# Optimization experiments

Measured on AMD Instinct MI355X. Metric: run time of the kernel, lower is better.

The kernel has to match this reference:

```python
import jax, jax.numpy as jnp
import numpy as np

B, D_IN, D_OUT, DICT = 2048, 768, 768, 24576
TOP_K, TOP_K_AUX = 32, 512
L1_COEFF, AUX_PENALTY, N_DEAD = 0.001, 0.03125, 100.0


def setup_inputs() -> dict:
    key = jax.random.key(0)
    k1, k2, k3, k4, k5, k6 = jax.random.split(key, 6)
    x_in = jax.random.normal(k1, (B, D_IN), dtype=jnp.float32)
    y_target = jax.random.normal(k2, (B, D_OUT), dtype=jnp.float32)
    nb = jax.random.randint(k3, (DICT,), 0, 200).astype(jnp.float32)
    # kaiming-uniform-ish init
    bound_e = float(np.sqrt(6.0 / D_IN))
    W_enc = jax.random.uniform(k4, (D_IN, DICT), minval=-bound_e, maxval=bound_e, dtype=jnp.float32)
    bound_d = float(np.sqrt(6.0 / DICT))
    W_dec = jax.random.uniform(k5, (DICT, D_OUT), minval=-bound_d, maxval=bound_d, dtype=jnp.float32)
    W_dec = W_dec / jnp.linalg.norm(W_dec, axis=-1, keepdims=True)  # unit-norm rows
    b_dec = jnp.zeros((D_OUT,), dtype=jnp.float32)
    return {"x_in": x_in, "y_target": y_target, "num_batches_not_active": nb,
            "W_enc": W_enc, "W_dec": W_dec, "b_dec": b_dec}


def _unit_norm(x):
    m = x.mean(axis=-1, keepdims=True)
    x = x - m
    s = jnp.std(x, axis=-1, keepdims=True, ddof=1)  # torch .std is unbiased
    return x / (s + 1e-5), m, s


def reference(x_in, y_target, num_batches_not_active, W_enc, W_dec, b_dec):
    xn, _, _ = _unit_norm(x_in)
    yn, y_mean, y_std = _unit_norm(y_target)
    x_enc = xn - b_dec  # pre_enc_bias (input_size == output_size)
    acts = jax.nn.relu(x_enc @ W_enc)                      # [B, DICT]
    vals, idx = jax.lax.top_k(acts, TOP_K)                 # [B, TOP_K]
    rows = jnp.arange(B)[:, None]
    acts_sparse = jnp.zeros_like(acts).at[rows, idx].set(vals)
    y_pred = acts_sparse @ W_dec + b_dec                   # [B, D_OUT]
    y_pred_out = y_pred * y_std + y_mean

    # stateful dead-feature bookkeeping (update_inactive_features)
    col_active = acts_sparse.sum(axis=0) > 0
    nb = jnp.where(col_active, 0.0, num_batches_not_active + 1.0)

    l2_loss = jnp.mean((y_pred - yn) ** 2)
    l1_norm = jnp.mean(jnp.abs(acts_sparse).sum(axis=-1))
    l1_loss = L1_COEFF * l1_norm
    l0_norm = jnp.mean((acts_sparse > 0).astype(jnp.float32).sum(axis=-1))

    # auxiliary loss on dead features (static-shape masked top-k; masked cols
    # get -1 < relu acts so extras relu-clip to 0 -> same math as torch gather)
    dead = nb >= N_DEAD
    masked = jnp.where(dead[None, :], acts, -1.0)
    av, ai = jax.lax.top_k(masked, TOP_K_AUX)
    av = jax.nn.relu(av)
    acts_aux = jnp.zeros_like(acts).at[rows, ai].set(av)
    y_pred_aux = acts_aux @ W_dec
    residual = yn - y_pred
    l2_aux = AUX_PENALTY * jnp.mean((y_pred_aux - residual) ** 2)
    aux_loss = jnp.where(dead.any(), l2_aux, 0.0)

    loss = l2_loss + l1_loss + aux_loss
    num_dead_features = (nb > N_DEAD).sum()
    return (y_pred_out, acts_sparse, loss, l2_loss, l1_loss, l0_norm, l1_norm,
            aux_loss, num_dead_features)
```

## Files before the change

kernel.cpp:

```cpp
#include <hip/hip_runtime.h>
#include <math.h>

#define BATCH 2048
#define DIN 768
#define DICT 24576
#define KM 32
#define KA 512
#define NPT 48
#define L1_COEFF 0.001f
#define AUX_PENALTY 0.03125f
#define CAND_MAX 128
#define CAND_DELTA 0.08f
#define AUXC (KA + 64)

typedef __attribute__((ext_vector_type(8))) short bf16x8;
typedef __attribute__((ext_vector_type(8))) unsigned short u16x8;
typedef __attribute__((ext_vector_type(4))) float f32x4;

constexpr size_t WS_XENC   = 0;
constexpr size_t WS_YN     = WS_XENC + (size_t)BATCH*DIN;
constexpr size_t WS_YMEAN  = WS_YN + (size_t)BATCH*DIN;
constexpr size_t WS_YSTD   = WS_YMEAN + BATCH;
constexpr size_t WS_RES    = WS_YSTD + BATCH;
constexpr size_t WS_NSEL   = WS_RES + (size_t)BATCH*DIN;
constexpr size_t WS_SEL    = WS_NSEL + BATCH;
constexpr size_t WS_SELV   = WS_SEL + (size_t)BATCH*KM;
constexpr size_t WS_COLACT = WS_SELV + (size_t)BATCH*KM;
constexpr size_t WS_ACC    = WS_COLACT + DICT;
constexpr size_t WS_DB     = WS_ACC + 8;
constexpr size_t WS_XEB    = WS_DB + DICT/32;
constexpr size_t WS_WETF   = WS_XEB + (size_t)BATCH*DIN/2;
constexpr size_t WS_WETB   = WS_WETF + (size_t)DICT*DIN;
constexpr size_t WS_WDB    = WS_WETB + (size_t)DICT*DIN/2;

__device__ __forceinline__ unsigned short f2b(float f){
    unsigned u = __float_as_uint(f);
    return (unsigned short)((u + 0x7fffu + ((u >> 16) & 1u)) >> 16);
}
__device__ __forceinline__ float b2f(unsigned short h){ return __uint_as_float(((unsigned)h) << 16); }

__device__ __forceinline__ void gld_lds16(const void* g, void* l){
    __builtin_amdgcn_global_load_lds(
        (const __attribute__((address_space(1))) unsigned int*)g,
        (__attribute__((address_space(3))) unsigned int*)l, 16, 0, 0);
}

__device__ __forceinline__ int blk_count512(int c, int* s16, int par){
    #pragma unroll
    for (int off=32; off; off>>=1) c += __shfl_down(c, off);
    if ((threadIdx.x & 63) == 0) s16[par*8 + (threadIdx.x >> 6)] = c;
    __syncthreads();
    int tot = 0;
    #pragma unroll
    for (int w=0; w<8; w++) tot += s16[par*8+w];
    return tot;
}
__device__ __forceinline__ float blk_sum512(float v, float* s16, int par){
    #pragma unroll
    for (int off=32; off; off>>=1) v += __shfl_down(v, off);
    if ((threadIdx.x & 63) == 0) s16[par*8 + (threadIdx.x >> 6)] = v;
    __syncthreads();
    float t = 0.f;
    #pragma unroll
    for (int w=0; w<8; w++) t += s16[par*8+w];
    return t;
}
__device__ __forceinline__ float blk_sum256(float v, float* s8, int par){
    #pragma unroll
    for (int off=32; off; off>>=1) v += __shfl_down(v, off);
    if ((threadIdx.x & 63) == 0) s8[par*4 + (threadIdx.x >> 6)] = v;
    __syncthreads();
    float t = 0.f;
    #pragma unroll
    for (int w=0; w<4; w++) t += s8[par*4+w];
    return t;
}

__global__ __launch_bounds__(256) void normalize_k(const float* __restrict__ x,
        const float* __restrict__ y, const float* __restrict__ bdec,
        float* __restrict__ ws){
    __shared__ float s8[8];
    int b = blockIdx.x; bool isy = b >= BATCH; int row = isy ? b - BATCH : b;
    const float* src = (isy ? y : x) + (size_t)row*DIN;
    int tid = threadIdx.x;
    float v0 = src[tid], v1 = src[tid+256], v2 = src[tid+512];
    float s = blk_sum256(v0+v1+v2, s8, 0);
    float mean = s * (1.f/(float)DIN);
    float d0 = v0-mean, d1 = v1-mean, d2 = v2-mean;
    float vs = blk_sum256(d0*d0+d1*d1+d2*d2, s8, 1);
    float sd = sqrtf(vs / (float)(DIN-1));
    float inv = 1.f / (sd + 1e-5f);
    if (isy){
        float* yn = ws + WS_YN + (size_t)row*DIN;
        yn[tid] = d0*inv; yn[tid+256] = d1*inv; yn[tid+512] = d2*inv;
        if (tid==0){ ws[WS_YMEAN+row] = mean; ws[WS_YSTD+row] = sd; }
    } else {
        float* xe = ws + WS_XENC + (size_t)row*DIN;
        unsigned short* xeb = (unsigned short*)(ws + WS_XEB) + (size_t)row*DIN;
        float e0 = d0*inv - bdec[tid];
        float e1 = d1*inv - bdec[tid+256];
        float e2 = d2*inv - bdec[tid+512];
        xe[tid] = e0; xe[tid+256] = e1; xe[tid+512] = e2;
        xeb[tid] = f2b(e0); xeb[tid+256] = f2b(e1); xeb[tid+512] = f2b(e2);
    }
}

__global__ __launch_bounds__(256) void transpose_k(const float* __restrict__ W,
        float* __restrict__ Tf, unsigned short* __restrict__ Tb){
    __shared__ float t[32][33];
    int n0 = blockIdx.x*32, k0 = blockIdx.y*32;
    int r = threadIdx.x >> 5, c = threadIdx.x & 31;
    #pragma unroll
    for (int rr=r; rr<32; rr+=8) t[rr][c] = W[(size_t)(k0+rr)*DICT + n0 + c];
    __syncthreads();
    #pragma unroll
    for (int rr=r; rr<32; rr+=8){
        float v = t[c][rr];
        Tf[(size_t)(n0+rr)*DIN + k0 + c] = v;
        Tb[(size_t)(n0+rr)*DIN + k0 + c] = f2b(v);
    }
}

__global__ __launch_bounds__(256) void wdecb_k(const float* __restrict__ W,
        unsigned short* __restrict__ Wb){
    size_t n4 = (size_t)DICT*DIN/4;
    for (size_t i = (size_t)blockIdx.x*256 + threadIdx.x; i < n4; i += (size_t)gridDim.x*256){
        float4 v = ((const float4*)W)[i];
        ushort4 o; o.x=f2b(v.x); o.y=f2b(v.y); o.z=f2b(v.z); o.w=f2b(v.w);
        ((ushort4*)Wb)[i] = o;
    }
}

__global__ __launch_bounds__(256) void gemm_mfma(const unsigned short* __restrict__ Abf,
        const unsigned short* __restrict__ Bbf, unsigned short* __restrict__ C){
    __shared__ __align__(16) unsigned short As[128*64];
    __shared__ __align__(16) unsigned short Bs[128*64];
    const int tid = threadIdx.x;
    const int w = tid >> 6, lane = tid & 63;
    const int m0 = blockIdx.y*128, n0 = blockIdx.x*128;
    const int srow = lane >> 3;
    const int schunk = (lane & 7) ^ srow;
    const int wm = (w >> 1)*64, wn = (w & 1)*64;
    f32x4 acc[16];
    #pragma unroll
    for (int i=0;i<16;i++) acc[i] = (f32x4){0.f,0.f,0.f,0.f};
    for (int kt = 0; kt < DIN; kt += 64){
        #pragma unroll
        for (int q=0;q<4;q++){
            int s = w*4 + q;
            int row = 8*s + srow;
            gld_lds16(Abf + (size_t)(m0+row)*DIN + kt + schunk*8, &As[8*s*64]);
            gld_lds16(Bbf + (size_t)(n0+row)*DIN + kt + schunk*8, &Bs[8*s*64]);
        }
        __syncthreads();
        #pragma unroll
        for (int kk=0; kk<64; kk+=32){
            bf16x8 af[4], bfr[4];
            int ch = (kk>>3) + (lane>>4);
            #pragma unroll
            for (int i=0;i<4;i++){
                int row = wm + i*16 + (lane&15);
                af[i] = *(const bf16x8*)&As[row*64 + ((ch ^ (row&7))<<3)];
            }
            #pragma unroll
            for (int j=0;j<4;j++){
                int row = wn + j*16 + (lane&15);
                bfr[j] = *(const bf16x8*)&Bs[row*64 + ((ch ^ (row&7))<<3)];
            }
            #pragma unroll
            for (int i=0;i<4;i++)
                #pragma unroll
                for (int j=0;j<4;j++)
                    acc[i*4+j] = __builtin_amdgcn_mfma_f32_16x16x32_bf16(af[i], bfr[j], acc[i*4+j], 0,0,0);
        }
        __syncthreads();
    }
    #pragma unroll
    for (int i=0;i<4;i++){
        #pragma unroll
        for (int r=0;r<4;r++){
            int m = m0 + wm + i*16 + (lane>>4)*4 + r;
            unsigned short* crow = C + (size_t)m*DICT + n0 + wn + (lane&15);
            #pragma unroll
            for (int j=0;j<4;j++)
                crow[j*16] = f2b(fmaxf(acc[i*4+j][r], 0.f) + 0.0f);
        }
    }
}

__global__ __launch_bounds__(512) void topk_main(const unsigned short* __restrict__ actsb,
        const float* __restrict__ WeTf, const float* __restrict__ Wdec,
        const float* __restrict__ bdec, float* __restrict__ ws,
        float* __restrict__ ypred_out){
    const int row = blockIdx.x, tid = threadIdx.x;
    const int lane = tid & 63, wid = tid >> 6;
    __shared__ int   s_i16[16];
    __shared__ float s_f16[16];
    __shared__ float s_x[DIN];
    __shared__ int   s_ci[CAND_MAX];
    __shared__ float s_cv[CAND_MAX];
    __shared__ int   s_li[KM];
    __shared__ float s_lv[KM];
    __shared__ int   s_n, s_m;
    const unsigned short* arow = actsb + (size_t)row * DICT;
    const float* xrow = ws + WS_XENC + (size_t)row * DIN;
    unsigned short h[NPT];
    #pragma unroll
    for (int i=0;i<6;i++){
        u16x8 v = *(const u16x8*)&arow[i*4096 + tid*8];
        #pragma unroll
        for (int e=0;e<8;e++) h[i*8+e] = v[e];
    }
    s_x[tid] = xrow[tid];
    if (tid < DIN-512) s_x[tid+512] = xrow[tid+512];
    if (tid == 0){ s_n = 0; s_m = 0; }

    int par = 0;
    unsigned prefix = 0;
    for (int bit=14; bit>=0; bit--){
        unsigned cand = prefix | (1u<<bit);
        int c = 0;
        #pragma unroll
        for (int q=0;q<NPT;q++) c += ((unsigned)h[q] >= cand) ? 1 : 0;
        int tot = blk_count512(c, s_i16, par); par ^= 1;
        if (tot >= KM) prefix = cand;
    }
    float tc = b2f((unsigned short)prefix) - CAND_DELTA;
    #pragma unroll
    for (int q=0;q<NPT;q++){
        if (b2f(h[q]) > tc){
            int p = atomicAdd(&s_n, 1);
            if (p < CAND_MAX) s_ci[p] = (q>>3)*4096 + tid*8 + (q&7);
        }
    }
    __syncthreads();
    int nc = s_n; if (nc > CAND_MAX) nc = CAND_MAX;
    for (int c = wid; c < nc; c += 8){
        const float* wr = WeTf + (size_t)s_ci[c]*DIN;
        float p = 0.f;
        #pragma unroll
        for (int t=0; t<12; t++) p = fmaf(s_x[lane + 64*t], wr[lane + 64*t], p);
        #pragma unroll
        for (int off=32; off; off>>=1) p += __shfl_down(p, off);
        if (lane == 0) s_cv[c] = fmaxf(p, 0.f);
    }
    __syncthreads();
    if (tid < nc){
        float vi = s_cv[tid]; int ii = s_ci[tid];
        int rank = 0;
        for (int j=0; j<nc; j++){
            float vj = s_cv[j];
            rank += (vj > vi) || (vj == vi && s_ci[j] < ii);
        }
        if (rank < KM){
            int p = atomicAdd(&s_m, 1);
            s_li[p] = ii; s_lv[p] = vi;
        }
    }
    __syncthreads();
    if (tid < KM){
        ((int*)ws)[WS_COLACT + s_li[tid]] = 1;
        ((int*)ws)[WS_SEL  + (size_t)row*KM + tid] = s_li[tid];
        ws[WS_SELV + (size_t)row*KM + tid] = s_lv[tid];
    }
    if (tid == 0){
        float l1 = 0.f; int l0 = 0;
        for (int l=0;l<KM;l++){ l1 += s_lv[l]; l0 += (s_lv[l] > 0.f); }
        atomicAdd(&ws[WS_ACC+1], l1);
        atomicAdd(&ws[WS_ACC+2], (float)l0);
    }
    __syncthreads();
    float ym = ws[WS_YMEAN+row], ys = ws[WS_YSTD+row];
    float l2loc = 0.f;
    for (int c = tid; c < DIN; c += 512){
        float acc = bdec[c];
        #pragma unroll 4
        for (int l=0;l<KM;l++) acc = fmaf(s_lv[l], Wdec[(size_t)s_li[l]*DIN + c], acc);
        float ynv = ws[WS_YN + (size_t)row*DIN + c];
        float d = acc - ynv;
        l2loc += d*d;
        ws[WS_RES + (size_t)row*DIN + c] = ynv - acc;
        ypred_out[(size_t)row*DIN + c] = fmaf(acc, ys, ym);
    }
    float l2t = blk_sum512(l2loc, s_f16, 0);
    if (tid==0) atomicAdd(&ws[WS_ACC+0], l2t);
}

__global__ __launch_bounds__(256) void dead_update(const float* __restrict__ nb,
        float* __restrict__ ws){
    int j = blockIdx.x*256 + threadIdx.x;
    int lane = threadIdx.x & 63;
    int act = ((const int*)ws)[WS_COLACT + j];
    float nbn = act ? 0.f : nb[j] + 1.f;
    bool dead = nbn >= 100.0f;
    unsigned long long bal = __ballot(dead ? 1 : 0);
    if (lane == 0){
        unsigned* db = (unsigned*)(ws + WS_DB);
        int w = j >> 5;
        db[w]   = (unsigned)bal;
        db[w+1] = (unsigned)(bal >> 32);
        if (bal) atomicOr(((int*)ws) + WS_ACC + 5, 1);
    }
    int c = (nbn > 100.0f) ? 1 : 0;
    #pragma unroll
    for (int off=32; off; off>>=1) c += __shfl_down(c, off);
    if (lane == 0 && c) atomicAdd(&ws[WS_ACC+4], (float)c);
}

__global__ __launch_bounds__(512) void aux_k(const unsigned short* __restrict__ actsb,
        const unsigned short* __restrict__ WdB, float* __restrict__ ws){
    const int row = blockIdx.x, tid = threadIdx.x;
    const int lane = tid & 63, wid = tid >> 6;
    __shared__ int      s_i16[16];
    __shared__ float    s_f16[16];
    __shared__ unsigned s_db[DICT/32];
    __shared__ int      s_li[AUXC];
    __shared__ float    s_lv[AUXC];
    __shared__ int      s_n;
    __shared__ float    s_red[8*DIN];
    const unsigned short* arow = actsb + (size_t)row * DICT;

    for (int i=tid; i<DICT/32; i+=512) s_db[i] = ((const unsigned*)(ws + WS_DB))[i];
    if (tid==0) s_n = 0;
    __syncthreads();

    unsigned short key[NPT];
    #pragma unroll
    for (int i=0;i<6;i++){
        u16x8 v = *(const u16x8*)&arow[i*4096 + tid*8];
        unsigned byte = (s_db[i*128 + (tid>>2)] >> ((tid&3)*8)) & 0xFFu;
        #pragma unroll
        for (int e=0;e<8;e++){
            unsigned short hv = v[e];
            key[i*8+e] = (((byte>>e)&1u) && hv) ? hv : 0;
        }
    }

    int par = 0;
    unsigned prefix = 0;
    for (int bit=14; bit>=0; bit--){
        unsigned cand = prefix | (1u<<bit);
        int c = 0;
        #pragma unroll
        for (int q=0;q<NPT;q++) c += ((unsigned)key[q] >= cand) ? 1 : 0;
        int tot = blk_count512(c, s_i16, par); par ^= 1;
        if (tot >= KA) prefix = cand;
    }
    unsigned thr = prefix ? prefix : 1u;
    #pragma unroll
    for (int q=0;q<NPT;q++){
        if ((unsigned)key[q] >= thr){
            int p = atomicAdd(&s_n, 1);
            if (p < AUXC){
                s_li[p] = (q>>3)*4096 + tid*8 + (q&7);
                s_lv[p] = b2f(key[q]);
            }
        }
    }
    __syncthreads();
    int n = s_n; if (n > AUXC) n = AUXC;

    float a[12];
    #pragma unroll
    for (int i=0;i<12;i++) a[i] = 0.f;
    const int base = lane*12;
    for (int l = wid; l < n; l += 8){
        float v = s_lv[l];
        const unsigned short* wr = WdB + (size_t)s_li[l]*DIN + base;
        ushort4 q0 = *(const ushort4*)wr;
        ushort4 q1 = *(const ushort4*)(wr+4);
        ushort4 q2 = *(const ushort4*)(wr+8);
        a[0] = fmaf(v, b2f(q0.x), a[0]); a[1] = fmaf(v, b2f(q0.y), a[1]);
        a[2] = fmaf(v, b2f(q0.z), a[2]); a[3] = fmaf(v, b2f(q0.w), a[3]);
        a[4] = fmaf(v, b2f(q1.x), a[4]); a[5] = fmaf(v, b2f(q1.y), a[5]);
        a[6] = fmaf(v, b2f(q1.z), a[6]); a[7] = fmaf(v, b2f(q1.w), a[7]);
        a[8] = fmaf(v, b2f(q2.x), a[8]); a[9] = fmaf(v, b2f(q2.y), a[9]);
        a[10]= fmaf(v, b2f(q2.z), a[10]); a[11]= fmaf(v, b2f(q2.w), a[11]);
    }
    float* pr = &s_red[wid*DIN + base];
    *(float4*)pr     = make_float4(a[0],a[1],a[2],a[3]);
    *(float4*)(pr+4) = make_float4(a[4],a[5],a[6],a[7]);
    *(float4*)(pr+8) = make_float4(a[8],a[9],a[10],a[11]);
    __syncthreads();
    float ss = 0.f;
    for (int c = tid; c < DIN; c += 512){
        float s = 0.f;
        #pragma unroll
        for (int w=0; w<8; w++) s += s_red[w*DIN + c];
        float d = s - ws[WS_RES + (size_t)row*DIN + c];
        ss += d*d;
    }
    float tot = blk_sum512(ss, s_f16, 0);
    if (tid==0) atomicAdd(&ws[WS_ACC+3], tot);
}

__global__ __launch_bounds__(256) void zscatter(const float* __restrict__ ws,
        float* __restrict__ acts){
    const int row = blockIdx.x, tid = threadIdx.x;
    float4 z = make_float4(0.f,0.f,0.f,0.f);
    float4* arow4 = (float4*)(acts + (size_t)row*DICT);
    #pragma unroll
    for (int i=0;i<24;i++) arow4[tid + 256*i] = z;
    __syncthreads();
    if (tid < KM){
        int j   = ((const int*)ws)[WS_SEL + (size_t)row*KM + tid];
        float v = ws[WS_SELV + (size_t)row*KM + tid];
        (acts + (size_t)row*DICT)[j] = v;
    }
}

__global__ void finalize_k(const float* __restrict__ ws, float* __restrict__ out){
    if (threadIdx.x == 0){
        float l2   = ws[WS_ACC+0] / (float)((size_t)BATCH*DIN);
        float l1n  = ws[WS_ACC+1] / (float)BATCH;
        float l1l  = L1_COEFF * l1n;
        float l0   = ws[WS_ACC+2] / (float)BATCH;
        float auxm = AUX_PENALTY * (ws[WS_ACC+3] / (float)((size_t)BATCH*DIN));
        int any    = ((const int*)ws)[WS_ACC+5];
        float auxl = any ? auxm : 0.f;
        out[0] = l2 + l1l + auxl;
        out[1] = l2;
        out[2] = l1l;
        out[3] = l0;
        out[4] = l1n;
        out[5] = auxl;
        out[6] = ws[WS_ACC+4];
    }
}

extern "C" void kernel_launch(void* const* d_in, const int* in_sizes, int n_in,
                              void* d_out, int out_size, void* d_ws, size_t ws_size,
                              hipStream_t stream){
    const float* x_in = (const float*)d_in[0];
    const float* y_t  = (const float*)d_in[1];
    const float* nb   = (const float*)d_in[2];
    const float* Wenc = (const float*)d_in[3];
    const float* Wdec = (const float*)d_in[4];
    const float* bdec = (const float*)d_in[5];
    float* out  = (float*)d_out;
    float* ws   = (float*)d_ws;
    float* acts = out + (size_t)BATCH*DIN;
    float* scal = out + (size_t)BATCH*DIN + (size_t)BATCH*DICT;
    unsigned short* actsb = (unsigned short*)acts;

    unsigned short* xeb  = (unsigned short*)(ws + WS_XEB);
    float*          wetf = ws + WS_WETF;
    unsigned short* wetb = (unsigned short*)(ws + WS_WETB);
    unsigned short* wdb  = (unsigned short*)(ws + WS_WDB);

    hipMemsetAsync(ws + WS_COLACT, 0, (DICT + 8) * sizeof(float), stream);
    normalize_k<<<2*BATCH, 256, 0, stream>>>(x_in, y_t, bdec, ws);
    transpose_k<<<dim3(DICT/32, DIN/32), 256, 0, stream>>>(Wenc, wetf, wetb);
    wdecb_k<<<2048, 256, 0, stream>>>(Wdec, wdb);
    gemm_mfma<<<dim3(DICT/128, BATCH/128), 256, 0, stream>>>(xeb, wetb, actsb);
    topk_main<<<BATCH, 512, 0, stream>>>(actsb, wetf, Wdec, bdec, ws, out);
    dead_update<<<DICT/256, 256, 0, stream>>>(nb, ws);
    aux_k<<<BATCH, 512, 0, stream>>>(actsb, wdb, ws);
    zscatter<<<BATCH, 256, 0, stream>>>(ws, acts);
    finalize_k<<<1, 64, 0, stream>>>(ws, scal);
}
```

Before: 838.9 us.

## Replace per-row aux gather-FMA with compacted dead-column MFMA GEMM

The auxiliary loss path now works only on dead columns. A prefix scan over the dead bitmask compacts both the per-row activations and a transposed bf16 W_dec down to those columns. The aux product then runs as a split-K MFMA GEMM that accumulates with atomics, followed by a separate loss-reduction kernel. This replaces the scattered per-row row-gathers of W_dec with dense tensor-core work. It adds several small kernels, a transpose and a memset, plus float atomic contention. The radix top-k count loops also switch to ballot/popcount wave counting.

Result: no change. 855.6 us (+2.0%).

```diff
diff --git a/kernel.cpp b/kernel.cpp
--- a/kernel.cpp
+++ b/kernel.cpp
@@ -11,7 +11,7 @@
 #define AUX_PENALTY 0.03125f
 #define CAND_MAX 128
 #define CAND_DELTA 0.08f
-#define AUXC (KA + 64)
+#define AUX_SPLIT 8
 
 typedef __attribute__((ext_vector_type(8))) short bf16x8;
 typedef __attribute__((ext_vector_type(8))) unsigned short u16x8;
@@ -32,6 +32,9 @@
 constexpr size_t WS_WETF   = WS_XEB + (size_t)BATCH*DIN/2;
 constexpr size_t WS_WETB   = WS_WETF + (size_t)DICT*DIN;
 constexpr size_t WS_WDB    = WS_WETB + (size_t)DICT*DIN/2;
+constexpr size_t WS_DCNT   = WS_XEB;
+constexpr size_t WS_DPREF  = WS_XEB + DICT/32;
+constexpr size_t WS_META   = WS_XEB + 2*(DICT/32);
 
 __device__ __forceinline__ unsigned short f2b(float f){
     unsigned u = __float_as_uint(f);
@@ -45,10 +48,8 @@
         (__attribute__((address_space(3))) unsigned int*)l, 16, 0, 0);
 }
 
-__device__ __forceinline__ int blk_count512(int c, int* s16, int par){
-    #pragma unroll
-    for (int off=32; off; off>>=1) c += __shfl_down(c, off);
-    if ((threadIdx.x & 63) == 0) s16[par*8 + (threadIdx.x >> 6)] = c;
+__device__ __forceinline__ int blk_count512_w(int cw, int* s16, int par){
+    if ((threadIdx.x & 63) == 0) s16[par*8 + (threadIdx.x >> 6)] = cw;
     __syncthreads();
     int tot = 0;
     #pragma unroll
@@ -121,14 +122,17 @@
     }
 }
 
-__global__ __launch_bounds__(256) void wdecb_k(const float* __restrict__ W,
-        unsigned short* __restrict__ Wb){
-    size_t n4 = (size_t)DICT*DIN/4;
-    for (size_t i = (size_t)blockIdx.x*256 + threadIdx.x; i < n4; i += (size_t)gridDim.x*256){
-        float4 v = ((const float4*)W)[i];
-        ushort4 o; o.x=f2b(v.x); o.y=f2b(v.y); o.z=f2b(v.z); o.w=f2b(v.w);
-        ((ushort4*)Wb)[i] = o;
-    }
+__global__ __launch_bounds__(256) void wdect_k(const float* __restrict__ W,
+        unsigned short* __restrict__ T){
+    __shared__ float t[32][33];
+    int j0 = blockIdx.x*32, n0 = blockIdx.y*32;
+    int r = threadIdx.x >> 5, c = threadIdx.x & 31;
+    #pragma unroll
+    for (int rr=r; rr<32; rr+=8) t[rr][c] = W[(size_t)(j0+rr)*DIN + n0 + c];
+    __syncthreads();
+    #pragma unroll
+    for (int rr=r; rr<32; rr+=8)
+        T[(size_t)(n0+rr)*DICT + j0 + c] = f2b(t[c][rr]);
 }
 
 __global__ __launch_bounds__(256) void gemm_mfma(const unsigned short* __restrict__ Abf,
@@ -221,8 +225,8 @@
         unsigned cand = prefix | (1u<<bit);
         int c = 0;
         #pragma unroll
-        for (int q=0;q<NPT;q++) c += ((unsigned)h[q] >= cand) ? 1 : 0;
-        int tot = blk_count512(c, s_i16, par); par ^= 1;
+        for (int q=0;q<NPT;q++) c += (int)__popcll(__ballot((unsigned)h[q] >= cand));
+        int tot = blk_count512_w(c, s_i16, par); par ^= 1;
         if (tot >= KM) prefix = cand;
     }
     float tc = b2f((unsigned short)prefix) - CAND_DELTA;
@@ -296,9 +300,12 @@
     unsigned long long bal = __ballot(dead ? 1 : 0);
     if (lane == 0){
         unsigned* db = (unsigned*)(ws + WS_DB);
+        int* dc = (int*)(ws + WS_DCNT);
         int w = j >> 5;
         db[w]   = (unsigned)bal;
         db[w+1] = (unsigned)(bal >> 32);
+        dc[w]   = __popc((unsigned)bal);
+        dc[w+1] = __popc((unsigned)(bal >> 32));
         if (bal) atomicOr(((int*)ws) + WS_ACC + 5, 1);
     }
     int c = (nbn > 100.0f) ? 1 : 0;
@@ -307,32 +314,91 @@
     if (lane == 0 && c) atomicAdd(&ws[WS_ACC+4], (float)c);
 }
 
-__global__ __launch_bounds__(512) void aux_k(const unsigned short* __restrict__ actsb,
-        const unsigned short* __restrict__ WdB, float* __restrict__ ws){
+__global__ __launch_bounds__(256) void scan_k(float* __restrict__ ws){
+    __shared__ int s[DICT/32];
+    const int* dc = (const int*)(ws + WS_DCNT);
+    int tid = threadIdx.x;
+    for (int i=tid; i<DICT/32; i+=256) s[i] = dc[i];
+    __syncthreads();
+    for (int off=1; off<DICT/32; off<<=1){
+        int v[3];
+        #pragma unroll
+        for (int k=0;k<3;k++){ int i = tid + 256*k; v[k] = (i >= off) ? s[i-off] : 0; }
+        __syncthreads();
+        #pragma unroll
+        for (int k=0;k<3;k++){ int i = tid + 256*k; s[i] += v[k]; }
+        __syncthreads();
+    }
+    int* dp = (int*)(ws + WS_DPREF);
+    for (int i=tid; i<DICT/32; i+=256) dp[i] = s[i] - dc[i];
+    if (tid == 0){
+        int nd = s[DICT/32 - 1];
+        int ndpad = (nd + 63) & ~63;
+        int nkt = ndpad >> 6;
+        int* meta = (int*)(ws + WS_META);
+        meta[0] = nd; meta[1] = ndpad; meta[2] = nkt;
+        meta[3] = (nkt + AUX_SPLIT - 1) / AUX_SPLIT;
+    }
+}
+
+__global__ __launch_bounds__(256) void wdtcompact_k(float* __restrict__ ws,
+        unsigned short* __restrict__ wdt){
+    __shared__ unsigned s_db[DICT/32];
+    __shared__ int      s_dp[DICT/32];
+    const int tid = threadIdx.x, n = blockIdx.x;
+    for (int i=tid; i<DICT/32; i+=256){
+        s_db[i] = ((const unsigned*)(ws + WS_DB))[i];
+        s_dp[i] = ((const int*)(ws + WS_DPREF))[i];
+    }
+    const int nd    = ((const int*)(ws + WS_META))[0];
+    const int ndpad = ((const int*)(ws + WS_META))[1];
+    __syncthreads();
+    unsigned short* row = wdt + (size_t)n*DICT;
+    for (int ch = 0; ch < DICT; ch += 4096){
+        unsigned short v[16];
+        u16x8 a = *(const u16x8*)&row[ch + tid*16];
+        u16x8 b = *(const u16x8*)&row[ch + tid*16 + 8];
+        #pragma unroll
+        for (int e=0;e<8;e++){ v[e] = a[e]; v[8+e] = b[e]; }
+        __syncthreads();
+        int w = (ch>>5) + (tid>>1);
+        unsigned dbw = s_db[w]; int dpw = s_dp[w];
+        int bit0 = (tid&1)*16;
+        #pragma unroll
+        for (int e=0;e<16;e++){
+            int bit = bit0 + e;
+            if ((dbw >> bit) & 1u)
+                row[dpw + __popc(dbw & ((1u<<bit)-1u))] = v[e];
+        }
+        __syncthreads();
+    }
+    for (int t = nd + tid; t < ndpad; t += 256) row[t] = 0;
+}
+
+__global__ __launch_bounds__(512) void aux_select(unsigned short* __restrict__ actsb,
+        float* __restrict__ ws){
     const int row = blockIdx.x, tid = threadIdx.x;
-    const int lane = tid & 63, wid = tid >> 6;
     __shared__ int      s_i16[16];
-    __shared__ float    s_f16[16];
     __shared__ unsigned s_db[DICT/32];
-    __shared__ int      s_li[AUXC];
-    __shared__ float    s_lv[AUXC];
-    __shared__ int      s_n;
-    __shared__ float    s_red[8*DIN];
-    const unsigned short* arow = actsb + (size_t)row * DICT;
-
-    for (int i=tid; i<DICT/32; i+=512) s_db[i] = ((const unsigned*)(ws + WS_DB))[i];
-    if (tid==0) s_n = 0;
+    __shared__ int      s_dp[DICT/32];
+    unsigned short* arow = actsb + (size_t)row * DICT;
+    for (int i=tid; i<DICT/32; i+=512){
+        s_db[i] = ((const unsigned*)(ws + WS_DB))[i];
+        s_dp[i] = ((const int*)(ws + WS_DPREF))[i];
+    }
+    const int nd    = ((const int*)(ws + WS_META))[0];
+    const int ndpad = ((const int*)(ws + WS_META))[1];
     __syncthreads();
 
     unsigned short key[NPT];
     #pragma unroll
     for (int i=0;i<6;i++){
         u16x8 v = *(const u16x8*)&arow[i*4096 + tid*8];
-        unsigned byte = (s_db[i*128 + (tid>>2)] >> ((tid&3)*8)) & 0xFFu;
+        unsigned dbw = s_db[i*128 + (tid>>2)];
         #pragma unroll
         for (int e=0;e<8;e++){
             unsigned short hv = v[e];
-            key[i*8+e] = (((byte>>e)&1u) && hv) ? hv : 0;
+            key[i*8+e] = (((dbw >> ((tid&3)*8 + e)) & 1u) && hv) ? hv : 0;
         }
     }
 
@@ -342,56 +408,107 @@
         unsigned cand = prefix | (1u<<bit);
         int c = 0;
         #pragma unroll
-        for (int q=0;q<NPT;q++) c += ((unsigned)key[q] >= cand) ? 1 : 0;
-        int tot = blk_count512(c, s_i16, par); par ^= 1;
+        for (int q=0;q<NPT;q++) c += (int)__popcll(__ballot((unsigned)key[q] >= cand));
+        int tot = blk_count512_w(c, s_i16, par); par ^= 1;
         if (tot >= KA) prefix = cand;
     }
     unsigned thr = prefix ? prefix : 1u;
-    #pragma unroll
-    for (int q=0;q<NPT;q++){
-        if ((unsigned)key[q] >= thr){
-            int p = atomicAdd(&s_n, 1);
-            if (p < AUXC){
-                s_li[p] = (q>>3)*4096 + tid*8 + (q&7);
-                s_lv[p] = b2f(key[q]);
+
+    #pragma unroll
+    for (int i=0;i<6;i++){
+        int w = i*128 + (tid>>2);
+        unsigned dbw = s_db[w];
+        int dpw = s_dp[w];
+        #pragma unroll
+        for (int e=0;e<8;e++){
+            int bit = (tid&3)*8 + e;
+            if ((dbw >> bit) & 1u){
+                int p = dpw + __popc(dbw & ((1u<<bit)-1u));
+                unsigned short kv = key[i*8+e];
+                arow[p] = ((unsigned)kv >= thr) ? kv : (unsigned short)0;
             }
         }
     }
-    __syncthreads();
-    int n = s_n; if (n > AUXC) n = AUXC;
-
-    float a[12];
-    #pragma unroll
-    for (int i=0;i<12;i++) a[i] = 0.f;
-    const int base = lane*12;
-    for (int l = wid; l < n; l += 8){
-        float v = s_lv[l];
-        const unsigned short* wr = WdB + (size_t)s_li[l]*DIN + base;
-        ushort4 q0 = *(const ushort4*)wr;
-        ushort4 q1 = *(const ushort4*)(wr+4);
-        ushort4 q2 = *(const ushort4*)(wr+8);
-        a[0] = fmaf(v, b2f(q0.x), a[0]); a[1] = fmaf(v, b2f(q0.y), a[1]);
-        a[2] = fmaf(v, b2f(q0.z), a[2]); a[3] = fmaf(v, b2f(q0.w), a[3]);
-        a[4] = fmaf(v, b2f(q1.x), a[4]); a[5] = fmaf(v, b2f(q1.y), a[5]);
-        a[6] = fmaf(v, b2f(q1.z), a[6]); a[7] = fmaf(v, b2f(q1.w), a[7]);
-        a[8] = fmaf(v, b2f(q2.x), a[8]); a[9] = fmaf(v, b2f(q2.y), a[9]);
-        a[10]= fmaf(v, b2f(q2.z), a[10]); a[11]= fmaf(v, b2f(q2.w), a[11]);
-    }
-    float* pr = &s_red[wid*DIN + base];
-    *(float4*)pr     = make_float4(a[0],a[1],a[2],a[3]);
-    *(float4*)(pr+4) = make_float4(a[4],a[5],a[6],a[7]);
-    *(float4*)(pr+8) = make_float4(a[8],a[9],a[10],a[11]);
-    __syncthreads();
-    float ss = 0.f;
-    for (int c = tid; c < DIN; c += 512){
-        float s = 0.f;
-        #pragma unroll
-        for (int w=0; w<8; w++) s += s_red[w*DIN + c];
-        float d = s - ws[WS_RES + (size_t)row*DIN + c];
-        ss += d*d;
-    }
-    float tot = blk_sum512(ss, s_f16, 0);
-    if (tid==0) atomicAdd(&ws[WS_ACC+3], tot);
+    for (int t = nd + tid; t < ndpad; t += 512) arow[t] = 0;
+}
+
+__global__ __launch_bounds__(256) void aux_gemm(const unsigned short* __restrict__ Abf,
+        const unsigned short* __restrict__ Bbf, const float* __restrict__ ws,
+        float* __restrict__ yaux){
+    const int nkt   = ((const int*)(ws + WS_META))[2];
+    const int chunk = ((const int*)(ws + WS_META))[3];
+    int t0 = blockIdx.z * chunk;
+    int t1 = t0 + chunk; if (t1 > nkt) t1 = nkt;
+    if (t0 >= t1) return;
+    __shared__ __align__(16) unsigned short As[128*64];
+    __shared__ __align__(16) unsigned short Bs[128*64];
+    const int tid = threadIdx.x;
+    const int w = tid >> 6, lane = tid & 63;
+    const int m0 = blockIdx.y*128, n0 = blockIdx.x*128;
+    const int srow = lane >> 3;
+    const int schunk = (lane & 7) ^ srow;
+    const int wm = (w >> 1)*64, wn = (w & 1)*64;
+    f32x4 acc[16];
+    #pragma unroll
+    for (int i=0;i<16;i++) acc[i] = (f32x4){0.f,0.f,0.f,0.f};
+    for (int t = t0; t < t1; ++t){
+        int kt = t*64;
+        #pragma unroll
+        for (int q=0;q<4;q++){
+            int s = w*4 + q;
+            int row = 8*s + srow;
+            gld_lds16(Abf + (size_t)(m0+row)*DICT + kt + schunk*8, &As[8*s*64]);
+            gld_lds16(Bbf + (size_t)(n0+row)*DICT + kt + schunk*8, &Bs[8*s*64]);
+        }
+        __syncthreads();
+        #pragma unroll
+        for (int kk=0; kk<64; kk+=32){
+            bf16x8 af[4], bfr[4];
+            int ch = (kk>>3) + (lane>>4);
+            #pragma unroll
+            for (int i=0;i<4;i++){
+                int row = wm + i*16 + (lane&15);
+                af[i] = *(const bf16x8*)&As[row*64 + ((ch ^ (row&7))<<3)];
+            }
+            #pragma unroll
+            for (int j=0;j<4;j++){
+                int row = wn + j*16 + (lane&15);
+                bfr[j] = *(const bf16x8*)&Bs[row*64 + ((ch ^ (row&7))<<3)];
+            }
+            #pragma unroll
+            for (int i=0;i<4;i++)
+                #pragma unroll
+                for (int j=0;j<4;j++)
+                    acc[i*4+j] = __builtin_amdgcn_mfma_f32_16x16x32_bf16(af[i], bfr[j], acc[i*4+j], 0,0,0);
+        }
+        __syncthreads();
+    }
+    #pragma unroll
+    for (int i=0;i<4;i++){
+        #pragma unroll
+        for (int r=0;r<4;r++){
+            int m = m0 + wm + i*16 + (lane>>4)*4 + r;
+            float* crow = yaux + (size_t)m*DIN + n0 + wn + (lane&15);
+            #pragma unroll
+            for (int j=0;j<4;j++) atomicAdd(&crow[j*16], acc[i*4+j][r]);
+        }
+    }
+}
+
+__global__ __launch_bounds__(256) void auxloss_k(const float* __restrict__ yaux,
+        float* __restrict__ ws){
+    __shared__ float s8[8];
+    const float4* y4 = (const float4*)yaux;
+    const float4* r4 = (const float4*)(ws + WS_RES);
+    float s = 0.f;
+    const size_t n4 = (size_t)BATCH*DIN/4;
+    for (size_t i = (size_t)blockIdx.x*256 + threadIdx.x; i < n4; i += (size_t)gridDim.x*256){
+        float4 a = y4[i], b = r4[i];
+        float d0 = a.x-b.x, d1 = a.y-b.y, d2 = a.z-b.z, d3 = a.w-b.w;
+        s += d0*d0 + d1*d1 + d2*d2 + d3*d3;
+    }
+    float tot = blk_sum256(s, s8, 0);
+    if (threadIdx.x == 0) atomicAdd(&ws[WS_ACC+3], tot);
 }
 
 __global__ __launch_bounds__(256) void zscatter(const float* __restrict__ ws,
@@ -446,16 +563,22 @@
     unsigned short* xeb  = (unsigned short*)(ws + WS_XEB);
     float*          wetf = ws + WS_WETF;
     unsigned short* wetb = (unsigned short*)(ws + WS_WETB);
-    unsigned short* wdb  = (unsigned short*)(ws + WS_WDB);
+    unsigned short* wdt  = (unsigned short*)(ws + WS_WDB);
+    float*          yaux = ws + WS_XENC;
 
     hipMemsetAsync(ws + WS_COLACT, 0, (DICT + 8) * sizeof(float), stream);
     normalize_k<<<2*BATCH, 256, 0, stream>>>(x_in, y_t, bdec, ws);
     transpose_k<<<dim3(DICT/32, DIN/32), 256, 0, stream>>>(Wenc, wetf, wetb);
-    wdecb_k<<<2048, 256, 0, stream>>>(Wdec, wdb);
+    wdect_k<<<dim3(DICT/32, DIN/32), 256, 0, stream>>>(Wdec, wdt);
     gemm_mfma<<<dim3(DICT/128, BATCH/128), 256, 0, stream>>>(xeb, wetb, actsb);
     topk_main<<<BATCH, 512, 0, stream>>>(actsb, wetf, Wdec, bdec, ws, out);
+    hipMemsetAsync(yaux, 0, (size_t)BATCH*DIN*sizeof(float), stream);
     dead_update<<<DICT/256, 256, 0, stream>>>(nb, ws);
-    aux_k<<<BATCH, 512, 0, stream>>>(actsb, wdb, ws);
+    scan_k<<<1, 256, 0, stream>>>(ws);
+    wdtcompact_k<<<DIN, 256, 0, stream>>>(ws, wdt);
+    aux_select<<<BATCH, 512, 0, stream>>>(actsb, ws);
+    aux_gemm<<<dim3(DIN/128, BATCH/128, AUX_SPLIT), 256, 0, stream>>>(actsb, wdt, ws, yaux);
+    auxloss_k<<<256, 256, 0, stream>>>(yaux, ws);
     zscatter<<<BATCH, 256, 0, stream>>>(ws, acts);
     finalize_k<<<1, 64, 0, stream>>>(ws, scal);
 }
```
